# Kernel tuning notes

Measured on AMD Instinct MI355X. Metric: run time of the kernel, lower is better.

## Reference

```python
import jax, jax.numpy as jnp
import numpy as np

# Module config (from init_kwargs)
B, S = 2, 2048            # batch, prompt length
NH, D = 16, 64            # num query heads, head_size
NKV = 4                   # num kv heads
QPK = NH // NKV           # queries per kv head (GQA)
BLOCK = 128               # paged KV-cache block size
NBLOCKS = 64              # total cache blocks
SCALE = 0.125             # 1/sqrt(D)
NEG = -1e9                # causal mask value (finite for grad safety)


def setup_inputs() -> dict:
    key = jax.random.key(0)
    k1, k2, k3 = jax.random.split(key, 3)
    query = jax.random.normal(k1, (B, S, NH * D), jnp.float32)
    key_t = jax.random.normal(k2, (B, S, NKV * D), jnp.float32)
    value = jax.random.normal(k3, (B, S, NKV * D), jnp.float32)
    # kv_cache = [2, num_blocks, block_size, num_kv_heads, head_size]
    kv_cache = jnp.zeros((2, NBLOCKS, BLOCK, NKV, D), jnp.float32)
    # causal attn_bias [B, 1, 1, S, S] as set by the vLLM model runner
    i = jnp.arange(S)
    causal = jnp.where(i[None, :] <= i[:, None], 0.0, NEG).astype(jnp.float32)
    attn_bias = jnp.broadcast_to(causal[None, None, None], (B, 1, 1, S, S))
    # standard alibi slopes for 16 heads: 2^(-0.5*(h+1))
    alibi_slopes = 2.0 ** (-0.5 * (jnp.arange(NH, dtype=jnp.float32) + 1.0))
    # prompt writes B*S/BLOCK = 32 full blocks into the cache
    block_indices = jnp.arange(B * S // BLOCK, dtype=jnp.int32)
    return {"query": query, "key": key_t, "value": value, "kv_cache": kv_cache,
            "attn_bias": attn_bias, "alibi_slopes": alibi_slopes,
            "block_indices": block_indices}


def reference(query, key, value, kv_cache, attn_bias, alibi_slopes, block_indices):
    Bq, Sq, _ = query.shape
    q = query.reshape(Bq, Sq, NKV, QPK, D)   # [b, i, h, g, d]
    k = key.reshape(Bq, Sq, NKV, D)          # [b, j, h, d]
    v = value.reshape(Bq, Sq, NKV, D)

    # --- paged KV-cache scatter (VLLMKVCache.insert_or_update_cache, prompt path) ---
    k_blocks = key.reshape(-1, BLOCK, NKV, D)   # [n_used_blocks, block, h, d]
    v_blocks = value.reshape(-1, BLOCK, NKV, D)
    key_cache = kv_cache[0].at[block_indices].set(k_blocks)
    value_cache = kv_cache[1].at[block_indices].set(v_blocks)

    # --- _make_alibi_bias: (j - i) * slope, unflattened to [1, Hkv, qpk, S, S] ---
    ar = jnp.arange(Sq)
    diff = (ar[None, :] - ar[:, None]).astype(query.dtype)        # [S, S]
    pos_bias = alibi_slopes[:, None, None] * diff                  # [NH, S, S]
    pos_bias = pos_bias.reshape(1, NKV, QPK, Sq, Sq)
    bias = attn_bias + pos_bias                                    # [B, Hkv, qpk, S, S]

    # --- prompt_attention: matmul_qk -> softmax -> matmul_av (GQA) ---
    scores = jnp.einsum('bihgd,bjhd->bhgij', q, k) * SCALE + bias
    attn = jax.nn.softmax(scores, axis=-1)
    out = jnp.einsum('bhgij,bjhd->bihgd', attn, v).reshape(Bq, Sq, NH * D)
    return out, key_cache, value_cache
```

## Files before the change

kernel.cpp:

```cpp
#include <hip/hip_runtime.h>
#include <hip/hip_bf16.h>
#include <math.h>

#define BB    2
#define SS    2048
#define NHh   16
#define DD    64
#define NKV   4
#define BLKV  128
#define SCALE 0.125f

#define QT   64
#define KT   64
#define LDP  72

typedef __attribute__((ext_vector_type(8))) short short8;
typedef __attribute__((ext_vector_type(4))) short short4v;
typedef __attribute__((ext_vector_type(4))) float f32x4;

__device__ inline short bf16c(float x) {
  __hip_bfloat16 h = __float2bfloat16(x);
  return *reinterpret_cast<short*>(&h);
}

#define GLL16(g, l) __builtin_amdgcn_global_load_lds( \
    (const __attribute__((address_space(1))) void*)(g), \
    (__attribute__((address_space(3))) void*)(l), 16, 0, 0)

__global__ __launch_bounds__(256) void aux_kernel(
    const float* __restrict__ k, const float* __restrict__ v,
    const float* __restrict__ kvc, const int* __restrict__ bidx, int nidx,
    unsigned short* __restrict__ kimg, unsigned short* __restrict__ vimg,
    float* __restrict__ kc, float* __restrict__ vc)
{
  const int wg = blockIdx.x;
  const int tid = threadIdx.x;
  if (wg < BB * NKV * (SS / KT)) {
    const int t   = wg & 31;
    const int hkv = (wg >> 5) & 3;
    const int b   = wg >> 7;
    const int j0  = t * KT;
    const float* kp = k + ((size_t)(b * SS + j0) * NKV + hkv) * DD;
    const float* vp = v + ((size_t)(b * SS + j0) * NKV + hkv) * DD;
    unsigned short* ki = kimg + (size_t)wg * 4096;
    unsigned short* vi = vimg + (size_t)wg * 4096;

    {
      const int jj = tid >> 2;
      const int sb = (tid & 3) * 2;
#pragma unroll
      for (int ss = 0; ss < 2; ++ss) {
        const int s  = sb + ss;
        const int d0 = (s ^ (jj & 7)) * 8;
        const float4 a = *(const float4*)(kp + jj * (NKV * DD) + d0);
        const float4 c = *(const float4*)(kp + jj * (NKV * DD) + d0 + 4);
        *(short8*)&ki[jj * 64 + s * 8] =
            (short8){bf16c(a.x), bf16c(a.y), bf16c(a.z), bf16c(a.w),
                     bf16c(c.x), bf16c(c.y), bf16c(c.z), bf16c(c.w)};
      }
    }
    {
      const int d = tid & 63;
      const int w = tid >> 6;
#pragma unroll
      for (int ji = 0; ji < 2; ++ji) {
        const int jb = w * 2 + ji;
        float vv[8];
#pragma unroll
        for (int e = 0; e < 8; ++e)
          vv[e] = vp[(jb * 8 + e) * (NKV * DD) + d];
        const int s = jb ^ (d & 7);
        *(short8*)&vi[d * 64 + s * 8] =
            (short8){bf16c(vv[0]), bf16c(vv[1]), bf16c(vv[2]), bf16c(vv[3]),
                     bf16c(vv[4]), bf16c(vv[5]), bf16c(vv[6]), bf16c(vv[7])};
      }
    }
  } else {
    const int cw    = wg - BB * NKV * (SS / KT);
    const int chunk = cw & 7;
    const int blk   = (cw >> 3) & 63;
    const int plane = cw >> 9;
    int src = -1;
    for (int m = 0; m < nidx; ++m) if (bidx[m] == blk) src = m;
    const float* sp;
    if (src >= 0) sp = (plane ? v : k) + (size_t)src * (BLKV * NKV * DD);
    else          sp = kvc + (size_t)plane * (64 * BLKV * NKV * DD)
                           + (size_t)blk * (BLKV * NKV * DD);
    float* dp = (plane ? vc : kc) + (size_t)blk * (BLKV * NKV * DD);
    const float4* s4 = (const float4*)sp + chunk * 1024;
    float4*       d4 = (float4*)dp + chunk * 1024;
#pragma unroll 4
    for (int i = tid; i < 1024; i += 256) d4[i] = s4[i];
  }
}

__global__ __launch_bounds__(256) void attn_kernel(
    const float* __restrict__ q, const unsigned short* __restrict__ kimg,
    const unsigned short* __restrict__ vimg, const float* __restrict__ slopes,
    float* __restrict__ out)
{
  __shared__ __align__(16) unsigned short Kbuf[2][4096];
  __shared__ __align__(16) unsigned short Vbuf[2][4096];
  __shared__ __align__(16) unsigned short P_lds[4][16 * LDP];
  __shared__ float sf_lds[4][16];

  const int tid  = threadIdx.x;
  const int wave = tid >> 6;
  const int lane = tid & 63;
  const int cl   = lane & 15;
  const int g    = lane >> 4;

  const int grp   = blockIdx.x & 7;
  const int b     = grp >> 2;
  const int hkv   = grp & 3;
  const int local = blockIdx.x >> 3;
  const int h     = hkv * 4 + (local & 3);
  const int qt    = 31 - (local >> 2);

  const float slope = slopes[h];
  const int q_blk = qt * QT;
  const int q0    = q_blk + wave * 16;
  const int iq    = q0 + cl;

  short8 qf[2];
  {
    const float* qp = q + ((size_t)(b * SS + q0 + cl) * NHh + h) * DD;
#pragma unroll
    for (int kq = 0; kq < 2; ++kq) {
      const int d0 = kq * 32 + g * 8;
      const float4 a = *(const float4*)(qp + d0);
      const float4 c = *(const float4*)(qp + d0 + 4);
      qf[kq] = (short8){bf16c(a.x), bf16c(a.y), bf16c(a.z), bf16c(a.w),
                        bf16c(c.x), bf16c(c.y), bf16c(c.z), bf16c(c.w)};
    }
  }

  float ab = slope * (float)(0 - iq);
  const float slope16 = slope * 16.f;
  const float slope64 = slope * 64.f;
  float cst[4];
#pragma unroll
  for (int r = 0; r < 4; ++r) cst[r] = slope * (float)(4 * g + r);

  float m = -INFINITY, l = 0.f;
  f32x4 acc[4];
#pragma unroll
  for (int dt = 0; dt < 4; ++dt) acc[dt] = (f32x4){0.f, 0.f, 0.f, 0.f};

  const char* kt0 = (const char*)kimg + (size_t)((b * NKV + hkv) * 32) * 8192;
  const char* vt0 = (const char*)vimg + (size_t)((b * NKV + hkv) * 32) * 8192;
  const int goff0 = (wave * 2) * 1024 + lane * 16;
  const int ldst0 = (wave * 2) * 1024;

  const int nt = qt + 1;
  int buf = 0;
  GLL16(kt0 + goff0,        (char*)&Kbuf[0][0] + ldst0);
  GLL16(kt0 + goff0 + 1024, (char*)&Kbuf[0][0] + ldst0 + 1024);
  GLL16(vt0 + goff0,        (char*)&Vbuf[0][0] + ldst0);
  GLL16(vt0 + goff0 + 1024, (char*)&Vbuf[0][0] + ldst0 + 1024);
  __syncthreads();

  for (int t = 0; t < nt; ++t) {
    if (t + 1 < nt) {
      const char* kt = kt0 + (size_t)(t + 1) * 8192;
      const char* vt = vt0 + (size_t)(t + 1) * 8192;
      GLL16(kt + goff0,        (char*)&Kbuf[buf ^ 1][0] + ldst0);
      GLL16(kt + goff0 + 1024, (char*)&Kbuf[buf ^ 1][0] + ldst0 + 1024);
      GLL16(vt + goff0,        (char*)&Vbuf[buf ^ 1][0] + ldst0);
      GLL16(vt + goff0 + 1024, (char*)&Vbuf[buf ^ 1][0] + ldst0 + 1024);
    }

    const unsigned short* Kb = Kbuf[buf];
    const unsigned short* Vb = Vbuf[buf];
    f32x4 sc[4];
    __builtin_amdgcn_s_setprio(1);
#pragma unroll
    for (int jt = 0; jt < 4; ++jt) {
      f32x4 s = (f32x4){0.f, 0.f, 0.f, 0.f};
#pragma unroll
      for (int kq = 0; kq < 2; ++kq) {
        const short8 kf = *(const short8*)
            &Kb[(jt * 16 + cl) * 64 + (((kq * 4 + g) ^ (cl & 7)) << 3)];
        s = __builtin_amdgcn_mfma_f32_16x16x32_bf16(kf, qf[kq], s, 0, 0, 0);
      }
      sc[jt] = s;
    }
    __builtin_amdgcn_s_setprio(0);

    const bool masked = (t == nt - 1);
    float pm = -INFINITY;
#pragma unroll
    for (int jt = 0; jt < 4; ++jt) {
      const float ajt = ab + slope16 * (float)jt;
#pragma unroll
      for (int r = 0; r < 4; ++r) {
        float val = fmaf(sc[jt][r], SCALE, ajt + cst[r]);
        if (masked) {
          const int j = t * 64 + jt * 16 + 4 * g + r;
          val = (j <= iq) ? val : -INFINITY;
        }
        sc[jt][r] = val;
        pm = fmaxf(pm, val);
      }
    }
    pm = fmaxf(pm, __shfl_xor(pm, 16));
    pm = fmaxf(pm, __shfl_xor(pm, 32));

    if (!__all(pm - m <= 8.f)) {
      const float mn = fmaxf(m, pm);
      const float sf = __expf(m - mn);
      m = mn;
      l *= sf;
      if (g == 0) sf_lds[wave][cl] = sf;
      asm volatile("s_waitcnt lgkmcnt(0)" ::: "memory");
      const f32x4 sfq = *(const f32x4*)&sf_lds[wave][4 * g];
#pragma unroll
      for (int dt = 0; dt < 4; ++dt)
#pragma unroll
        for (int r = 0; r < 4; ++r) acc[dt][r] *= sfq[r];
    }

    float rs = 0.f;
#pragma unroll
    for (int jt = 0; jt < 4; ++jt) {
      const float p0 = __expf(sc[jt][0] - m);
      const float p1 = __expf(sc[jt][1] - m);
      const float p2 = __expf(sc[jt][2] - m);
      const float p3 = __expf(sc[jt][3] - m);
      rs += p0 + p1 + p2 + p3;
      *(short4v*)&P_lds[wave][cl * LDP + jt * 16 + 4 * g] =
          (short4v){bf16c(p0), bf16c(p1), bf16c(p2), bf16c(p3)};
    }
    rs += __shfl_xor(rs, 16);
    rs += __shfl_xor(rs, 32);
    l += rs;

    asm volatile("s_waitcnt lgkmcnt(0)" ::: "memory");

    __builtin_amdgcn_s_setprio(1);
#pragma unroll
    for (int ks = 0; ks < 2; ++ks) {
      const short8 pa = *(const short8*)&P_lds[wave][cl * LDP + ks * 32 + g * 8];
#pragma unroll
      for (int dt = 0; dt < 4; ++dt) {
        const short8 vb = *(const short8*)
            &Vb[(dt * 16 + cl) * 64 + (((ks * 4 + g) ^ (cl & 7)) << 3)];
        acc[dt] = __builtin_amdgcn_mfma_f32_16x16x32_bf16(pa, vb, acc[dt], 0, 0, 0);
      }
    }
    __builtin_amdgcn_s_setprio(0);

    __syncthreads();
    buf ^= 1;
    ab += slope64;
  }

  if (g == 0) sf_lds[wave][cl] = l;
  asm volatile("s_waitcnt lgkmcnt(0)" ::: "memory");
  const f32x4 lq = *(const f32x4*)&sf_lds[wave][4 * g];
#pragma unroll
  for (int r = 0; r < 4; ++r) {
    const float inv = 1.f / lq[r];
    float* op = out + ((size_t)(b * SS + q0 + 4 * g + r) * NHh + h) * DD;
#pragma unroll
    for (int dt = 0; dt < 4; ++dt) op[dt * 16 + cl] = acc[dt][r] * inv;
  }
}

extern "C" void kernel_launch(void* const* d_in, const int* in_sizes, int n_in,
                              void* d_out, int out_size, void* d_ws, size_t ws_size,
                              hipStream_t stream) {
  const float* q      = (const float*)d_in[0];
  const float* k      = (const float*)d_in[1];
  const float* v      = (const float*)d_in[2];
  const float* kvc    = (const float*)d_in[3];
  const float* slopes = (const float*)d_in[5];
  const int*   bidx   = (const int*)d_in[6];

  float* out = (float*)d_out;
  float* kc  = out + BB * SS * NHh * DD;
  float* vc  = kc + 64 * BLKV * NKV * DD;

  unsigned short* kimg = (unsigned short*)d_ws;
  unsigned short* vimg = kimg + (size_t)BB * NKV * 32 * 4096;

  const int nidx = in_sizes[6];

  aux_kernel<<<dim3(256 + 1024), dim3(256), 0, stream>>>(
      k, v, kvc, bidx, nidx, kimg, vimg, kc, vc);

  attn_kernel<<<dim3(BB * NHh * (SS / QT)), dim3(256), 0, stream>>>(
      q, kimg, vimg, slopes, out);
}
```

Before: 60.56 us.

## Map waves to GQA heads sharing K/V tile and fuse cache scatter into conversion

After: 91.56 us. +51.2%, slower.

```diff
diff --git a/kernel.cpp b/kernel.cpp
--- a/kernel.cpp
+++ b/kernel.cpp
@@ -10,9 +10,9 @@
 #define BLKV  128
 #define SCALE 0.125f
 
-#define QT   64
-#define KT   64
-#define LDP  72
+#define KT    64
+#define QTH   32
+#define LDP   72
 
 typedef __attribute__((ext_vector_type(8))) short short8;
 typedef __attribute__((ext_vector_type(4))) short short4v;
@@ -33,7 +33,7 @@
     unsigned short* __restrict__ kimg, unsigned short* __restrict__ vimg,
     float* __restrict__ kc, float* __restrict__ vc)
 {
-  const int wg = blockIdx.x;
+  const int wg  = blockIdx.x;
   const int tid = threadIdx.x;
   if (wg < BB * NKV * (SS / KT)) {
     const int t   = wg & 31;
@@ -44,6 +44,10 @@
     const float* vp = v + ((size_t)(b * SS + j0) * NKV + hkv) * DD;
     unsigned short* ki = kimg + (size_t)wg * 4096;
     unsigned short* vi = vimg + (size_t)wg * 4096;
+    const int bi    = bidx[b * 16 + (t >> 1)];
+    const int rowc0 = (t & 1) * 64;
+    float* kcb = kc + (size_t)bi * (BLKV * NKV * DD);
+    float* vcb = vc + (size_t)bi * (BLKV * NKV * DD);
 
     {
       const int jj = tid >> 2;
@@ -57,6 +61,9 @@
         *(short8*)&ki[jj * 64 + s * 8] =
             (short8){bf16c(a.x), bf16c(a.y), bf16c(a.z), bf16c(a.w),
                      bf16c(c.x), bf16c(c.y), bf16c(c.z), bf16c(c.w)};
+        float* kd = kcb + (rowc0 + jj) * (NKV * DD) + hkv * DD + d0;
+        *(float4*)kd       = a;
+        *(float4*)(kd + 4) = c;
       }
     }
     {
@@ -73,24 +80,23 @@
         *(short8*)&vi[d * 64 + s * 8] =
             (short8){bf16c(vv[0]), bf16c(vv[1]), bf16c(vv[2]), bf16c(vv[3]),
                      bf16c(vv[4]), bf16c(vv[5]), bf16c(vv[6]), bf16c(vv[7])};
+#pragma unroll
+        for (int e = 0; e < 8; ++e)
+          vcb[(rowc0 + jb * 8 + e) * (NKV * DD) + hkv * DD + d] = vv[e];
       }
     }
   } else {
-    const int cw    = wg - BB * NKV * (SS / KT);
-    const int chunk = cw & 7;
-    const int blk   = (cw >> 3) & 63;
-    const int plane = cw >> 9;
-    int src = -1;
-    for (int m = 0; m < nidx; ++m) if (bidx[m] == blk) src = m;
-    const float* sp;
-    if (src >= 0) sp = (plane ? v : k) + (size_t)src * (BLKV * NKV * DD);
-    else          sp = kvc + (size_t)plane * (64 * BLKV * NKV * DD)
-                           + (size_t)blk * (BLKV * NKV * DD);
-    float* dp = (plane ? vc : kc) + (size_t)blk * (BLKV * NKV * DD);
-    const float4* s4 = (const float4*)sp + chunk * 1024;
-    float4*       d4 = (float4*)dp + chunk * 1024;
+    const int w2    = wg - BB * NKV * (SS / KT);
+    const int blk   = w2 & 63;
+    const int plane = w2 >> 6;
+    int covered = 0;
+    for (int m = 0; m < nidx; ++m) covered |= (bidx[m] == blk);
+    if (covered) return;
+    const float4* s4 = (const float4*)(kvc + (size_t)plane * (64 * BLKV * NKV * DD)
+                                           + (size_t)blk * (BLKV * NKV * DD));
+    float4* d4 = (float4*)((plane ? vc : kc) + (size_t)blk * (BLKV * NKV * DD));
 #pragma unroll 4
-    for (int i = tid; i < 1024; i += 256) d4[i] = s4[i];
+    for (int i = tid; i < (BLKV * NKV * DD) / 4; i += 256) d4[i] = s4[i];
   }
 }
 
@@ -101,8 +107,8 @@
 {
   __shared__ __align__(16) unsigned short Kbuf[2][4096];
   __shared__ __align__(16) unsigned short Vbuf[2][4096];
-  __shared__ __align__(16) unsigned short P_lds[4][16 * LDP];
-  __shared__ float sf_lds[4][16];
+  __shared__ __align__(16) unsigned short P_lds[4][2][16 * LDP];
+  __shared__ float sf_lds[4][2][16];
 
   const int tid  = threadIdx.x;
   const int wave = tid >> 6;
@@ -110,49 +116,52 @@
   const int cl   = lane & 15;
   const int g    = lane >> 4;
 
-  const int grp   = blockIdx.x & 7;
-  const int b     = grp >> 2;
-  const int hkv   = grp & 3;
-  const int local = blockIdx.x >> 3;
-  const int h     = hkv * 4 + (local & 3);
-  const int qt    = 31 - (local >> 2);
+  const int grp = blockIdx.x & 7;
+  const int b   = grp >> 2;
+  const int hkv = grp & 3;
+  const int qt  = 63 - (blockIdx.x >> 3);
+  const int h   = hkv * 4 + wave;
 
   const float slope = slopes[h];
-  const int q_blk = qt * QT;
-  const int q0    = q_blk + wave * 16;
-  const int iq    = q0 + cl;
-
-  short8 qf[2];
-  {
-    const float* qp = q + ((size_t)(b * SS + q0 + cl) * NHh + h) * DD;
+  const int q0 = qt * QTH;
+  const int nt = qt / 2 + 1;
+
+  short8 qf[2][2];
+#pragma unroll
+  for (int f = 0; f < 2; ++f) {
+    const float* qp = q + ((size_t)(b * SS + q0 + 16 * f + cl) * NHh + h) * DD;
 #pragma unroll
     for (int kq = 0; kq < 2; ++kq) {
       const int d0 = kq * 32 + g * 8;
       const float4 a = *(const float4*)(qp + d0);
       const float4 c = *(const float4*)(qp + d0 + 4);
-      qf[kq] = (short8){bf16c(a.x), bf16c(a.y), bf16c(a.z), bf16c(a.w),
-                        bf16c(c.x), bf16c(c.y), bf16c(c.z), bf16c(c.w)};
-    }
-  }
-
-  float ab = slope * (float)(0 - iq);
+      qf[f][kq] = (short8){bf16c(a.x), bf16c(a.y), bf16c(a.z), bf16c(a.w),
+                           bf16c(c.x), bf16c(c.y), bf16c(c.z), bf16c(c.w)};
+    }
+  }
+
   const float slope16 = slope * 16.f;
   const float slope64 = slope * 64.f;
+  float ab[2];
+#pragma unroll
+  for (int f = 0; f < 2; ++f) ab[f] = -slope * (float)(q0 + 16 * f + cl);
   float cst[4];
 #pragma unroll
   for (int r = 0; r < 4; ++r) cst[r] = slope * (float)(4 * g + r);
 
-  float m = -INFINITY, l = 0.f;
-  f32x4 acc[4];
-#pragma unroll
-  for (int dt = 0; dt < 4; ++dt) acc[dt] = (f32x4){0.f, 0.f, 0.f, 0.f};
+  float m_[2] = {-INFINITY, -INFINITY};
+  float l_[2] = {0.f, 0.f};
+  f32x4 acc[2][4];
+#pragma unroll
+  for (int f = 0; f < 2; ++f)
+#pragma unroll
+    for (int dt = 0; dt < 4; ++dt) acc[f][dt] = (f32x4){0.f, 0.f, 0.f, 0.f};
 
   const char* kt0 = (const char*)kimg + (size_t)((b * NKV + hkv) * 32) * 8192;
   const char* vt0 = (const char*)vimg + (size_t)((b * NKV + hkv) * 32) * 8192;
-  const int goff0 = (wave * 2) * 1024 + lane * 16;
-  const int ldst0 = (wave * 2) * 1024;
-
-  const int nt = qt + 1;
+  const int goff0 = wave * 2048 + lane * 16;
+  const int ldst0 = wave * 2048;
+
   int buf = 0;
   GLL16(kt0 + goff0,        (char*)&Kbuf[0][0] + ldst0);
   GLL16(kt0 + goff0 + 1024, (char*)&Kbuf[0][0] + ldst0 + 1024);
@@ -169,101 +178,116 @@
       GLL16(vt + goff0,        (char*)&Vbuf[buf ^ 1][0] + ldst0);
       GLL16(vt + goff0 + 1024, (char*)&Vbuf[buf ^ 1][0] + ldst0 + 1024);
     }
-
     const unsigned short* Kb = Kbuf[buf];
     const unsigned short* Vb = Vbuf[buf];
-    f32x4 sc[4];
+    const bool masked = (t == nt - 1);
+
+    f32x4 sc[2][4];
     __builtin_amdgcn_s_setprio(1);
 #pragma unroll
     for (int jt = 0; jt < 4; ++jt) {
-      f32x4 s = (f32x4){0.f, 0.f, 0.f, 0.f};
-#pragma unroll
-      for (int kq = 0; kq < 2; ++kq) {
-        const short8 kf = *(const short8*)
-            &Kb[(jt * 16 + cl) * 64 + (((kq * 4 + g) ^ (cl & 7)) << 3)];
-        s = __builtin_amdgcn_mfma_f32_16x16x32_bf16(kf, qf[kq], s, 0, 0, 0);
-      }
-      sc[jt] = s;
+      const int rb = (jt * 16 + cl) * 64;
+      const short8 kfA = *(const short8*)&Kb[rb + ((g       ^ (cl & 7)) << 3)];
+      const short8 kfB = *(const short8*)&Kb[rb + (((4 | g) ^ (cl & 7)) << 3)];
+#pragma unroll
+      for (int f = 0; f < 2; ++f) {
+        f32x4 s = (f32x4){0.f, 0.f, 0.f, 0.f};
+        s = __builtin_amdgcn_mfma_f32_16x16x32_bf16(kfA, qf[f][0], s, 0, 0, 0);
+        s = __builtin_amdgcn_mfma_f32_16x16x32_bf16(kfB, qf[f][1], s, 0, 0, 0);
+        sc[f][jt] = s;
+      }
     }
     __builtin_amdgcn_s_setprio(0);
 
-    const bool masked = (t == nt - 1);
-    float pm = -INFINITY;
-#pragma unroll
-    for (int jt = 0; jt < 4; ++jt) {
-      const float ajt = ab + slope16 * (float)jt;
-#pragma unroll
-      for (int r = 0; r < 4; ++r) {
-        float val = fmaf(sc[jt][r], SCALE, ajt + cst[r]);
-        if (masked) {
-          const int j = t * 64 + jt * 16 + 4 * g + r;
-          val = (j <= iq) ? val : -INFINITY;
+#pragma unroll
+    for (int f = 0; f < 2; ++f) {
+      const int iq = q0 + 16 * f + cl;
+      float pm = -INFINITY;
+#pragma unroll
+      for (int jt = 0; jt < 4; ++jt) {
+        const float ajt = ab[f] + slope16 * (float)jt;
+#pragma unroll
+        for (int r = 0; r < 4; ++r) {
+          float val = fmaf(sc[f][jt][r], SCALE, ajt + cst[r]);
+          if (masked) {
+            const int j = t * 64 + jt * 16 + 4 * g + r;
+            val = (j <= iq) ? val : -INFINITY;
+          }
+          sc[f][jt][r] = val;
+          pm = fmaxf(pm, val);
         }
-        sc[jt][r] = val;
-        pm = fmaxf(pm, val);
-      }
-    }
-    pm = fmaxf(pm, __shfl_xor(pm, 16));
-    pm = fmaxf(pm, __shfl_xor(pm, 32));
-
-    if (!__all(pm - m <= 8.f)) {
-      const float mn = fmaxf(m, pm);
-      const float sf = __expf(m - mn);
-      m = mn;
-      l *= sf;
-      if (g == 0) sf_lds[wave][cl] = sf;
-      asm volatile("s_waitcnt lgkmcnt(0)" ::: "memory");
-      const f32x4 sfq = *(const f32x4*)&sf_lds[wave][4 * g];
-#pragma unroll
-      for (int dt = 0; dt < 4; ++dt)
-#pragma unroll
-        for (int r = 0; r < 4; ++r) acc[dt][r] *= sfq[r];
-    }
-
-    float rs = 0.f;
-#pragma unroll
-    for (int jt = 0; jt < 4; ++jt) {
-      const float p0 = __expf(sc[jt][0] - m);
-      const float p1 = __expf(sc[jt][1] - m);
-      const float p2 = __expf(sc[jt][2] - m);
-      const float p3 = __expf(sc[jt][3] - m);
-      rs += p0 + p1 + p2 + p3;
-      *(short4v*)&P_lds[wave][cl * LDP + jt * 16 + 4 * g] =
-          (short4v){bf16c(p0), bf16c(p1), bf16c(p2), bf16c(p3)};
-    }
-    rs += __shfl_xor(rs, 16);
-    rs += __shfl_xor(rs, 32);
-    l += rs;
+      }
+      pm = fmaxf(pm, __shfl_xor(pm, 16));
+      pm = fmaxf(pm, __shfl_xor(pm, 32));
+
+      if (!__all(pm - m_[f] <= 8.f)) {
+        const float mn = fmaxf(m_[f], pm);
+        const float sf = __expf(m_[f] - mn);
+        m_[f] = mn;
+        l_[f] *= sf;
+        if (g == 0) sf_lds[wave][f][cl] = sf;
+        asm volatile("s_waitcnt lgkmcnt(0)" ::: "memory");
+        const f32x4 sfq = *(const f32x4*)&sf_lds[wave][f][4 * g];
+#pragma unroll
+        for (int dt = 0; dt < 4; ++dt)
+#pragma unroll
+          for (int r = 0; r < 4; ++r) acc[f][dt][r] *= sfq[r];
+      }
+
+      float rs = 0.f;
+#pragma unroll
+      for (int jt = 0; jt < 4; ++jt) {
+        const float p0 = __expf(sc[f][jt][0] - m_[f]);
+        const float p1 = __expf(sc[f][jt][1] - m_[f]);
+        const float p2 = __expf(sc[f][jt][2] - m_[f]);
+        const float p3 = __expf(sc[f][jt][3] - m_[f]);
+        rs += p0 + p1 + p2 + p3;
+        *(short4v*)&P_lds[wave][f][cl * LDP + jt * 16 + 4 * g] =
+            (short4v){bf16c(p0), bf16c(p1), bf16c(p2), bf16c(p3)};
+      }
+      rs += __shfl_xor(rs, 16);
+      rs += __shfl_xor(rs, 32);
+      l_[f] += rs;
+    }
 
     asm volatile("s_waitcnt lgkmcnt(0)" ::: "memory");
 
     __builtin_amdgcn_s_setprio(1);
 #pragma unroll
     for (int ks = 0; ks < 2; ++ks) {
-      const short8 pa = *(const short8*)&P_lds[wave][cl * LDP + ks * 32 + g * 8];
+      const short8 pa0 = *(const short8*)&P_lds[wave][0][cl * LDP + ks * 32 + g * 8];
+      const short8 pa1 = *(const short8*)&P_lds[wave][1][cl * LDP + ks * 32 + g * 8];
 #pragma unroll
       for (int dt = 0; dt < 4; ++dt) {
         const short8 vb = *(const short8*)
-            &Vb[(dt * 16 + cl) * 64 + (((ks * 4 + g) ^ (cl & 7)) << 3)];
-        acc[dt] = __builtin_amdgcn_mfma_f32_16x16x32_bf16(pa, vb, acc[dt], 0, 0, 0);
+            &Vb[(dt * 16 + cl) * 64 + ((((ks << 2) | g) ^ (cl & 7)) << 3)];
+        acc[0][dt] = __builtin_amdgcn_mfma_f32_16x16x32_bf16(pa0, vb, acc[0][dt], 0, 0, 0);
+        acc[1][dt] = __builtin_amdgcn_mfma_f32_16x16x32_bf16(pa1, vb, acc[1][dt], 0, 0, 0);
       }
     }
     __builtin_amdgcn_s_setprio(0);
 
     __syncthreads();
     buf ^= 1;
-    ab += slope64;
-  }
-
-  if (g == 0) sf_lds[wave][cl] = l;
+    ab[0] += slope64;
+    ab[1] += slope64;
+  }
+
+#pragma unroll
+  for (int f = 0; f < 2; ++f) {
+    if (g == 0) sf_lds[wave][f][cl] = l_[f];
+  }
   asm volatile("s_waitcnt lgkmcnt(0)" ::: "memory");
-  const f32x4 lq = *(const f32x4*)&sf_lds[wave][4 * g];
-#pragma unroll
-  for (int r = 0; r < 4; ++r) {
-    const float inv = 1.f / lq[r];
-    float* op = out + ((size_t)(b * SS + q0 + 4 * g + r) * NHh + h) * DD;
-#pragma unroll
-    for (int dt = 0; dt < 4; ++dt) op[dt * 16 + cl] = acc[dt][r] * inv;
+#pragma unroll
+  for (int f = 0; f < 2; ++f) {
+    const f32x4 lq = *(const f32x4*)&sf_lds[wave][f][4 * g];
+#pragma unroll
+    for (int r = 0; r < 4; ++r) {
+      const float inv = 1.f / lq[r];
+      float* op = out + ((size_t)(b * SS + q0 + 16 * f + 4 * g + r) * NHh + h) * DD;
+#pragma unroll
+      for (int dt = 0; dt < 4; ++dt) op[dt * 16 + cl] = acc[f][dt][r] * inv;
+    }
   }
 }
 
@@ -286,9 +310,8 @@
 
   const int nidx = in_sizes[6];
 
-  aux_kernel<<<dim3(256 + 1024), dim3(256), 0, stream>>>(
+  aux_kernel<<<dim3(256 + 128), dim3(256), 0, stream>>>(
       k, v, kvc, bidx, nidx, kimg, vimg, kc, vc);
 
-  attn_kernel<<<dim3(BB * NHh * (SS / QT)), dim3(256), 0, stream>>>(
-      q, kimg, vimg, slopes, out);
+  attn_kernel<<<dim3(512), dim3(256), 0, stream>>>(q, kimg, vimg, slopes, out);
 }
```
